# Performance work log

Hardware: AMD Instinct MI355X
Metric: run time of the kernel (lower is better)

The kernel has to match this reference:

```python
import jax, jax.numpy as jnp
import numpy as np

DIM = 512
HEADS = 8
HEAD_DIM = DIM // HEADS
EPS = 1e-6
LN_EPS = 1e-5


def setup_inputs() -> dict:
    key = jax.random.key(0)
    ks = jax.random.split(key, 7)
    B, S = 2, 2048
    std = 1.0 / np.sqrt(DIM)
    return {
        "x": jax.random.normal(ks[0], (B, S, DIM), dtype=jnp.float32),
        "Wq": jax.random.normal(ks[1], (DIM, DIM), dtype=jnp.float32) * std,
        "Wk": jax.random.normal(ks[2], (DIM, DIM), dtype=jnp.float32) * std,
        "Wv": jax.random.normal(ks[3], (DIM, DIM), dtype=jnp.float32) * std,
        "Wo": jax.random.normal(ks[4], (DIM, DIM), dtype=jnp.float32) * std,
        "ln_gamma": jnp.ones((DIM,), dtype=jnp.float32),
        "ln_beta": jnp.zeros((DIM,), dtype=jnp.float32),
    }


def _hardsigmoid(x):
    return jnp.clip(x / 6.0 + 0.5, 0.0, 1.0)


def _softshrink(x, lambd=0.5):
    return jnp.where(x > lambd, x - lambd, jnp.where(x < -lambd, x + lambd, 0.0))


def reference(x, Wq, Wk, Wv, Wo, ln_gamma, ln_beta):
    B, S, D = x.shape
    # torch Linear: y = x @ W.T
    q = (x @ Wq.T).reshape(B, S, HEADS, HEAD_DIM).transpose(0, 2, 1, 3)
    k = (x @ Wk.T).reshape(B, S, HEADS, HEAD_DIM).transpose(0, 2, 1, 3)
    v = (x @ Wv.T).reshape(B, S, HEADS, HEAD_DIM).transpose(0, 2, 1, 3)
    scale = 1.0 / np.sqrt(HEAD_DIM)
    scores = jnp.einsum("bhqd,bhkd->bhqk", q, k) * scale  # [B,H,S,S]
    attn_soft = jax.nn.softmax(scores, axis=-1)
    gated = attn_soft * _hardsigmoid(scores)
    attn_weights = gated / (gated.sum(axis=-1, keepdims=True) + EPS)
    attn_out = jnp.einsum("bhqk,bhkd->bhqd", attn_weights, v)
    attn_out = attn_out.transpose(0, 2, 1, 3).reshape(B, S, D)
    out = attn_out @ Wo.T
    out = out / (1.0 + jnp.abs(out))  # softsign
    out = out + _softshrink(x)
    # LayerNorm over last dim
    mu = out.mean(axis=-1, keepdims=True)
    var = ((out - mu) ** 2).mean(axis=-1, keepdims=True)
    out = (out - mu) * jax.lax.rsqrt(var + LN_EPS) * ln_gamma + ln_beta
    return out
```

## Files before the change

### kernel.cpp

```cpp
#include <hip/hip_runtime.h>

#define DIMD 512
#define NB 2
#define SEQ 2048
#define NHEADS 8
#define HDIM 64
#define MROWS (NB*SEQ)

typedef short s16x8 __attribute__((ext_vector_type(8)));
typedef float f32x4 __attribute__((ext_vector_type(4)));
typedef float f32x16 __attribute__((ext_vector_type(16)));
typedef unsigned short u16;
typedef unsigned int u32;

__device__ __forceinline__ u16 f2bf(float f) {
    union { float f; u32 u; } c; c.f = f;
    u32 u = c.u;
    return (u16)((u + 0x7FFFu + ((u >> 16) & 1u)) >> 16);
}
__device__ __forceinline__ float bf2f(u16 v) {
    union { u32 u; float f; } c; c.u = ((u32)v) << 16;
    return c.f;
}

__device__ __forceinline__ f32x4 mfma16(s16x8 a, s16x8 b, f32x4 c) {
    return __builtin_amdgcn_mfma_f32_16x16x32_bf16(a, b, c, 0, 0, 0);
}
__device__ __forceinline__ f32x16 mfma32(s16x8 a, s16x8 b, f32x16 c) {
    return __builtin_amdgcn_mfma_f32_32x32x16_bf16(a, b, c, 0, 0, 0);
}

#define GLDS16(g, l) __builtin_amdgcn_global_load_lds( \
    (const __attribute__((address_space(1))) void*)(g), \
    (__attribute__((address_space(3))) void*)(l), 16, 0, 0)

#define ESCF 0.180336880111f
#define HSC2 0.115524530f

__global__ void cvt_all(const float* __restrict__ x, const float* __restrict__ Wq,
                        const float* __restrict__ Wk, const float* __restrict__ Wv,
                        const float* __restrict__ Wo,
                        u16* __restrict__ xb, u16* __restrict__ wqkv, u16* __restrict__ wo) {
    int i = blockIdx.x * blockDim.x + threadIdx.x;
    const float* src; u16* dst; int idx;
    if (i < 524288) { src = x; dst = xb; idx = i; }
    else {
        int jj = i - 524288;
        int which = jj >> 16; idx = jj & 65535;
        src = which == 0 ? Wq : which == 1 ? Wk : which == 2 ? Wv : Wo;
        dst = which < 3 ? wqkv + which*DIMD*DIMD : wo;
    }
    float4 v = reinterpret_cast<const float4*>(src)[idx];
    ushort4 o;
    o.x = f2bf(v.x); o.y = f2bf(v.y); o.z = f2bf(v.z); o.w = f2bf(v.w);
    reinterpret_cast<ushort4*>(dst)[idx] = o;
}

template<int WMODE>
__global__ __launch_bounds__(256) void gemm128(const u16* __restrict__ A, const u16* __restrict__ Bm,
                                               void* __restrict__ Cout, void* __restrict__ Cout2,
                                               void* __restrict__ Cout3, int M, int N, int K) {
    __shared__ u16 As[128*64];
    __shared__ u16 Bs[128*64];
    const int bm0 = blockIdx.x * 128, bn0 = blockIdx.y * 128;
    const int t = threadIdx.x;
    const int w = t >> 6, l = t & 63;
    const int lg = l >> 4, lr = l & 15;
    const int wm = w >> 1, wn = w & 1;
    f32x4 acc[4][4] = {};
    const int srow = w*32 + (l >> 3);
    const int swc = ((l & 7) ^ ((l >> 3) & 7)) * 8;
    const u16* asrc = A  + (size_t)(bm0 + srow)*K + swc;
    const u16* bsrc = Bm + (size_t)(bn0 + srow)*K + swc;
    const int ldsb = w*2048;

    for (int k0 = 0; k0 < K; k0 += 64) {
        #pragma unroll
        for (int g = 0; g < 4; g++) {
            GLDS16(asrc + (size_t)g*8*K + k0, &As[ldsb + g*512]);
            GLDS16(bsrc + (size_t)g*8*K + k0, &Bs[ldsb + g*512]);
        }
        __syncthreads();
        #pragma unroll
        for (int ks = 0; ks < 2; ks++) {
            const int swr = ((ks*4 + lg) ^ (lr & 7)) * 8;
            s16x8 af[4], bfr[4];
            #pragma unroll
            for (int fm = 0; fm < 4; fm++)
                af[fm] = *(const s16x8*)&As[(wm*64 + fm*16 + lr)*64 + swr];
            #pragma unroll
            for (int fn = 0; fn < 4; fn++)
                bfr[fn] = *(const s16x8*)&Bs[(wn*64 + fn*16 + lr)*64 + swr];
            #pragma unroll
            for (int fm = 0; fm < 4; fm++)
                #pragma unroll
                for (int fn = 0; fn < 4; fn++)
                    acc[fm][fn] = mfma16(af[fm], bfr[fn], acc[fm][fn]);
        }
        __syncthreads();
    }

    const int region = (WMODE == 3) ? (bn0 >> 9) : 0;
    const float qsc = (WMODE == 3 && region == 0) ? ESCF : 1.0f;
    #pragma unroll
    for (int fm = 0; fm < 4; fm++) {
        #pragma unroll
        for (int fn = 0; fn < 4; fn++) {
            const int mb = bm0 + wm*64 + fm*16 + lg*4;
            const int n  = bn0 + wn*64 + fn*16 + lr;
            if (WMODE == 2) {
                float* C = (float*)Cout;
                #pragma unroll
                for (int i = 0; i < 4; i++)
                    C[(size_t)(mb + i)*N + n] = acc[fm][fn][i];
            } else {
                const int nl = n & 511;
                if (region == 2) {
                    const int b = mb >> 11, s0 = mb & 2047;
                    const int h = nl >> 6, d = nl & 63;
                    ushort4 pk;
                    pk.x = f2bf(acc[fm][fn][0]);
                    pk.y = f2bf(acc[fm][fn][1]);
                    pk.z = f2bf(acc[fm][fn][2]);
                    pk.w = f2bf(acc[fm][fn][3]);
                    *(ushort4*)((u16*)Cout3 + (size_t)((b*8 + h)*64 + d)*2048 + s0) = pk;
                } else {
                    u16* C = region == 0 ? (u16*)Cout : (u16*)Cout2;
                    #pragma unroll
                    for (int i = 0; i < 4; i++)
                        C[(size_t)(mb + i)*512 + nl] = f2bf(acc[fm][fn][i] * qsc);
                }
            }
        }
    }
}

__global__ __launch_bounds__(256) void gemm_bt2(const u16* __restrict__ A, const u16* __restrict__ Bm,
                                                u16* __restrict__ Cout, int M, int N, int K) {
    __shared__ u16 As[64*64];
    __shared__ u16 Bs[64*64];
    const int bm0 = blockIdx.x * 64, bn0 = blockIdx.y * 64;
    const int t = threadIdx.x;
    const int w = t >> 6, l = t & 63;
    const int lg = l >> 4, lr = l & 15;
    const int wm = w >> 1, wn = w & 1;
    f32x4 acc[2][2] = {};
    const int srow = t >> 3;
    const int scol = (t & 7) * 8;

    for (int k0 = 0; k0 < K; k0 += 64) {
        #pragma unroll
        for (int c = 0; c < 2; c++) {
            const u16* ga = A  + (size_t)(bm0 + c*32 + srow)*K + k0 + scol;
            const u16* gb = Bm + (size_t)(bn0 + c*32 + srow)*K + k0 + scol;
            GLDS16(ga, (char*)As + c*4096 + w*1024);
            GLDS16(gb, (char*)Bs + c*4096 + w*1024);
        }
        __syncthreads();
        #pragma unroll
        for (int ks = 0; ks < 2; ks++) {
            s16x8 af[2], bfr[2];
            #pragma unroll
            for (int fm = 0; fm < 2; fm++)
                af[fm] = *(const s16x8*)&As[(wm*32 + fm*16 + lr)*64 + ks*32 + lg*8];
            #pragma unroll
            for (int fn = 0; fn < 2; fn++)
                bfr[fn] = *(const s16x8*)&Bs[(wn*32 + fn*16 + lr)*64 + ks*32 + lg*8];
            #pragma unroll
            for (int fm = 0; fm < 2; fm++)
                #pragma unroll
                for (int fn = 0; fn < 2; fn++)
                    acc[fm][fn] = mfma16(af[fm], bfr[fn], acc[fm][fn]);
        }
        __syncthreads();
    }

    #pragma unroll
    for (int fm = 0; fm < 2; fm++)
        #pragma unroll
        for (int fn = 0; fn < 2; fn++) {
            const int mb = bm0 + wm*32 + fm*16 + lg*4;
            const int n  = bn0 + wn*32 + fn*16 + lr;
            #pragma unroll
            for (int i = 0; i < 4; i++)
                Cout[(size_t)(mb + i)*N + n] = f2bf(acc[fm][fn][i]);
        }
}

__device__ __forceinline__ void attn_phase32(const u16* Kc, const u16* Vc, const s16x8* qf,
                                             f32x16& o0, f32x16& o1, float& gacc,
                                             int ln, int hi, int l7) {
    #pragma unroll
    for (int kb = 0; kb < 4; kb++) {
        f32x16 sc = {};
        __builtin_amdgcn_s_setprio(1);
        #pragma unroll
        for (int c = 0; c < 4; c++) {
            s16x8 kf = *(const s16x8*)&Kc[(kb*32 + ln)*64 + (((c << 1) | hi) ^ l7)*8];
            sc = mfma32(kf, qf[c], sc);
        }
        __builtin_amdgcn_s_setprio(0);
        u32 u[4][2];
        #pragma unroll
        for (int b2 = 0; b2 < 4; b2++) {
            float ww[4];
            #pragma unroll
            for (int r = 0; r < 4; r++) {
                const float s = sc[b2*4 + r];
                const float e = exp2f(s);
                const float hs = __builtin_amdgcn_fmed3f(s*HSC2 + 0.5f, 0.f, 1.f);
                ww[r] = e*hs;
            }
            gacc += (ww[0] + ww[1]) + (ww[2] + ww[3]);
            asm("v_cvt_pk_bf16_f32 %0, %1, %2" : "=v"(u[b2][0]) : "v"(ww[0]), "v"(ww[1]));
            asm("v_cvt_pk_bf16_f32 %0, %1, %2" : "=v"(u[b2][1]) : "v"(ww[2]), "v"(ww[3]));
        }
        #pragma unroll
        for (int c16 = 0; c16 < 2; c16++) {
            u32 x0 = u[2*c16][0], y0 = u[2*c16+1][0];
            u32 x1 = u[2*c16][1], y1 = u[2*c16+1][1];
            asm("v_permlane32_swap_b32 %0, %1" : "+v"(x0), "+v"(y0));
            asm("v_permlane32_swap_b32 %0, %1" : "+v"(x1), "+v"(y1));
            union { u32 uu[4]; s16x8 v; } pa;
            pa.uu[0] = x0; pa.uu[1] = x1; pa.uu[2] = y0; pa.uu[3] = y1;
            const int ccv = kb*4 + c16*2 + hi;
            s16x8 vf0 = *(const s16x8*)&Vc[(size_t)ln*128        + (ccv ^ l7)*8];
            s16x8 vf1 = *(const s16x8*)&Vc[(size_t)(32 + ln)*128 + (ccv ^ l7)*8];
            __builtin_amdgcn_s_setprio(1);
            o0 = mfma32(pa.v, vf0, o0);
            o1 = mfma32(pa.v, vf1, o1);
            __builtin_amdgcn_s_setprio(0);
        }
    }
}

__global__ __launch_bounds__(256) void attn_split(const u16* __restrict__ q, const u16* __restrict__ k,
                                                  const u16* __restrict__ vt,
                                                  float* __restrict__ opart, float* __restrict__ gpart) {
    __shared__ u16 Ks[2][128*64];
    __shared__ u16 Vs[2][64*128];
    const int bid = blockIdx.x;
    const int xcd = bid & 7, j = bid >> 3;
    const int g4 = j >> 4, qt = j & 15;
    const int bhks = xcd*4 + g4;
    const int bh = bhks >> 1, ks = bhks & 1;
    const int b = bh >> 3, h = bh & 7;
    const int qb0 = qt * 128;
    const int t = threadIdx.x;
    const int w = t >> 6, l = t & 63;
    const int ln = l & 31, hi = l >> 5, l7 = l & 7;

    const size_t qrow = (size_t)(b*SEQ + qb0 + w*32 + ln);
    s16x8 qf[4];
    #pragma unroll
    for (int c = 0; c < 4; c++)
        qf[c] = *(const s16x8*)(q + qrow*DIMD + h*HDIM + c*16 + hi*8);

    const int srow = w*32 + (l >> 3);
    const int kswc = (l7 ^ (l >> 3)) * 8;
    const u16* ksrc = k + (size_t)(b*SEQ + ks*1024 + srow)*DIMD + h*HDIM + kswc;
    const u16* vbase = vt + (size_t)bh*HDIM*SEQ + ks*1024;
    int voff[4];
    #pragma unroll
    for (int g = 0; g < 4; g++) {
        const int vrow = w*16 + g*4 + (l >> 4);
        const int vc = ((l & 15) ^ (vrow & 7)) * 8;
        voff[g] = vrow*SEQ + vc;
    }
    const int ldsb = w*2048;

    f32x16 o0 = {}, o1 = {};
    float gacc = 0.f;

    #pragma unroll
    for (int g = 0; g < 4; g++) {
        GLDS16(ksrc + (size_t)g*8*DIMD, &Ks[0][ldsb + g*512]);
        GLDS16(vbase + voff[g],          &Vs[0][ldsb + g*512]);
    }
    __syncthreads();

    #pragma unroll 1
    for (int tp = 0; tp < 4; ++tp) {
        const int tt0 = tp*2;
        {
            const size_t adv = (size_t)(tt0 + 1) * 128;
            #pragma unroll
            for (int g = 0; g < 4; g++) {
                GLDS16(ksrc + (adv + g*8)*DIMD, &Ks[1][ldsb + g*512]);
                GLDS16(vbase + voff[g] + adv,   &Vs[1][ldsb + g*512]);
            }
        }
        attn_phase32(&Ks[0][0], &Vs[0][0], qf, o0, o1, gacc, ln, hi, l7);
        __syncthreads();
        if (tp < 3) {
            const size_t adv = (size_t)(tt0 + 2) * 128;
            #pragma unroll
            for (int g = 0; g < 4; g++) {
                GLDS16(ksrc + (adv + g*8)*DIMD, &Ks[0][ldsb + g*512]);
                GLDS16(vbase + voff[g] + adv,   &Vs[0][ldsb + g*512]);
            }
        }
        attn_phase32(&Ks[1][0], &Vs[1][0], qf, o0, o1, gacc, ln, hi, l7);
        __syncthreads();
    }

    gacc += __shfl_xor(gacc, 32);
    if (l < 32)
        gpart[((size_t)ks*16 + bh)*SEQ + qb0 + w*32 + l] = gacc;

    float* op = opart + ((size_t)ks*MROWS + b*SEQ + qb0 + w*32)*DIMD + h*HDIM;
    #pragma unroll
    for (int i = 0; i < 16; i++) {
        const int qr = (i & 3) + 8*(i >> 2) + 4*hi;
        op[(size_t)qr*DIMD + ln]      = o0[i];
        op[(size_t)qr*DIMD + 32 + ln] = o1[i];
    }
}

__global__ __launch_bounds__(256) void attn_combine(const float* __restrict__ opart,
                                                    const float* __restrict__ gpart,
                                                    u16* __restrict__ attn) {
    const int idx = blockIdx.x*256 + threadIdx.x;
    const int row = idx >> 7;
    const int col = (idx & 127) * 4;
    const int b = row >> 11, s = row & 2047, h = col >> 6;
    const float g = gpart[((size_t)(b*8 + h))*SEQ + s]
                  + gpart[((size_t)(16 + b*8 + h))*SEQ + s];
    const float inv = 1.f / g;
    const float4 a0 = *(const float4*)(opart + (size_t)row*DIMD + col);
    const float4 a1 = *(const float4*)(opart + ((size_t)MROWS + row)*DIMD + col);
    ushort4 r;
    r.x = f2bf((a0.x + a1.x)*inv);
    r.y = f2bf((a0.y + a1.y)*inv);
    r.z = f2bf((a0.z + a1.z)*inv);
    r.w = f2bf((a0.w + a1.w)*inv);
    *(ushort4*)(attn + (size_t)row*DIMD + col) = r;
}

__global__ __launch_bounds__(256) void ln_epilogue(const u16* __restrict__ proj, const float* __restrict__ x,
                                                   const float* __restrict__ gamma, const float* __restrict__ beta,
                                                   float* __restrict__ out) {
    const int row = blockIdx.x*4 + (threadIdx.x >> 6);
    const int l = threadIdx.x & 63;
    const u16* pr = proj + (size_t)row*DIMD + l*8;
    const float* xr = x  + (size_t)row*DIMD + l*8;
    s16x8 pv = *(const s16x8*)pr;
    float tv[8];
    float s = 0.f, s2 = 0.f;
    #pragma unroll
    for (int j = 0; j < 2; j++) {
        float4 xv = *(const float4*)(xr + j*4);
        float xa[4] = {xv.x, xv.y, xv.z, xv.w};
        #pragma unroll
        for (int qq = 0; qq < 4; qq++) {
            const float p = bf2f((u16)pv[j*4+qq]);
            const float ss = p / (1.f + fabsf(p));
            const float xx = xa[qq];
            const float sh = xx > 0.5f ? xx - 0.5f : (xx < -0.5f ? xx + 0.5f : 0.f);
            const float tt = ss + sh;
            tv[j*4+qq] = tt; s += tt; s2 += tt*tt;
        }
    }
    #pragma unroll
    for (int m = 1; m < 64; m <<= 1) { s += __shfl_xor(s, m); s2 += __shfl_xor(s2, m); }
    const float mu = s * (1.f/512.f);
    float var = s2 * (1.f/512.f) - mu*mu;
    const float rstd = rsqrtf(var + 1e-5f);
    #pragma unroll
    for (int j = 0; j < 2; j++) {
        float4 g  = *(const float4*)(gamma + l*8 + j*4);
        float4 bb = *(const float4*)(beta  + l*8 + j*4);
        float4 ov;
        ov.x = (tv[j*4+0]-mu)*rstd*g.x + bb.x;
        ov.y = (tv[j*4+1]-mu)*rstd*g.y + bb.y;
        ov.z = (tv[j*4+2]-mu)*rstd*g.z + bb.z;
        ov.w = (tv[j*4+3]-mu)*rstd*g.w + bb.w;
        *(float4*)(out + (size_t)row*DIMD + l*8 + j*4) = ov;
    }
}

extern "C" void kernel_launch(void* const* d_in, const int* in_sizes, int n_in,
                              void* d_out, int out_size, void* d_ws, size_t ws_size,
                              hipStream_t stream) {
    const float* x     = (const float*)d_in[0];
    const float* Wq    = (const float*)d_in[1];
    const float* Wk    = (const float*)d_in[2];
    const float* Wv    = (const float*)d_in[3];
    const float* Wo    = (const float*)d_in[4];
    const float* gamma = (const float*)d_in[5];
    const float* beta  = (const float*)d_in[6];
    float* out = (float*)d_out;
    char* ws = (char*)d_ws;

    u16* xb    = (u16*)(ws);
    u16* wqkvb = (u16*)(ws + (4<<20));
    u16* wob   = (u16*)(ws + (4<<20) + (1536<<10));
    u16* qb    = (u16*)(ws + (6<<20));
    u16* kb    = (u16*)(ws + (10<<20));
    u16* vtb   = (u16*)(ws + (14<<20));
    u16* ab    = (u16*)(ws + (18<<20));
    u16* proj  = (u16*)(ws + (22<<20));
    float* opart = (float*)(ws + (26<<20));
    float* gpart = (float*)(ws + (42<<20));

    cvt_all<<<3072, 256, 0, stream>>>(x, Wq, Wk, Wv, Wo, xb, wqkvb, wob);

    gemm128<3><<<dim3(MROWS/128, 1536/128), 256, 0, stream>>>(xb, wqkvb, qb, kb, vtb, MROWS, 1536, DIMD);

    attn_split<<<512, 256, 0, stream>>>(qb, kb, vtb, opart, gpart);
    attn_combine<<<2048, 256, 0, stream>>>(opart, gpart, ab);

    gemm_bt2<<<dim3(MROWS/64, DIMD/64), 256, 0, stream>>>(ab, wob, proj, MROWS, DIMD, DIMD);

    ln_epilogue<<<MROWS/4, 256, 0, stream>>>(proj, x, gamma, beta, out);
}
```

Measured before the change: 76.95 us.

## Split attention keys four ways with smaller tiles and bf16 partial outputs

Moves the attention split-K from 2 to 4 key partitions. Each block now processes 512 keys in 64-key tiles, which halves the LDS footprint, and 1024 blocks are launched instead of 512. Partial outputs are stored as bf16 rather than fp32 to cut the write and read traffic into the combine kernel, which now sums four partitions. The aim is more parallelism and occupancy, at the cost of per-block startup overhead, extra partial data to combine, and lower precision in the partial sums.

```diff
diff --git a/kernel.cpp b/kernel.cpp
--- a/kernel.cpp
+++ b/kernel.cpp
@@ -187,11 +187,11 @@
         }
 }
 
-__device__ __forceinline__ void attn_phase32(const u16* Kc, const u16* Vc, const s16x8* qf,
+__device__ __forceinline__ void attn_phase64(const u16* Kc, const u16* Vc, const s16x8* qf,
                                              f32x16& o0, f32x16& o1, float& gacc,
                                              int ln, int hi, int l7) {
     #pragma unroll
-    for (int kb = 0; kb < 4; kb++) {
+    for (int kb = 0; kb < 2; kb++) {
         f32x16 sc = {};
         __builtin_amdgcn_s_setprio(1);
         #pragma unroll
@@ -224,8 +224,8 @@
             union { u32 uu[4]; s16x8 v; } pa;
             pa.uu[0] = x0; pa.uu[1] = x1; pa.uu[2] = y0; pa.uu[3] = y1;
             const int ccv = kb*4 + c16*2 + hi;
-            s16x8 vf0 = *(const s16x8*)&Vc[(size_t)ln*128        + (ccv ^ l7)*8];
-            s16x8 vf1 = *(const s16x8*)&Vc[(size_t)(32 + ln)*128 + (ccv ^ l7)*8];
+            s16x8 vf0 = *(const s16x8*)&Vc[(size_t)ln*64        + (ccv ^ l7)*8];
+            s16x8 vf1 = *(const s16x8*)&Vc[(size_t)(32 + ln)*64 + (ccv ^ l7)*8];
             __builtin_amdgcn_s_setprio(1);
             o0 = mfma32(pa.v, vf0, o0);
             o1 = mfma32(pa.v, vf1, o1);
@@ -236,14 +236,14 @@
 
 __global__ __launch_bounds__(256) void attn_split(const u16* __restrict__ q, const u16* __restrict__ k,
                                                   const u16* __restrict__ vt,
-                                                  float* __restrict__ opart, float* __restrict__ gpart) {
-    __shared__ u16 Ks[2][128*64];
-    __shared__ u16 Vs[2][64*128];
+                                                  u16* __restrict__ opart, float* __restrict__ gpart) {
+    __shared__ u16 Ks[2][64*64];
+    __shared__ u16 Vs[2][64*64];
     const int bid = blockIdx.x;
     const int xcd = bid & 7, j = bid >> 3;
-    const int g4 = j >> 4, qt = j & 15;
-    const int bhks = xcd*4 + g4;
-    const int bh = bhks >> 1, ks = bhks & 1;
+    const int g8 = j >> 4, qt = j & 15;
+    const int bhks = xcd*8 + g8;
+    const int bh = bhks >> 2, ks = bhks & 3;
     const int b = bh >> 3, h = bh & 7;
     const int qb0 = qt * 128;
     const int t = threadIdx.x;
@@ -256,26 +256,19 @@
     for (int c = 0; c < 4; c++)
         qf[c] = *(const s16x8*)(q + qrow*DIMD + h*HDIM + c*16 + hi*8);
 
-    const int srow = w*32 + (l >> 3);
-    const int kswc = (l7 ^ (l >> 3)) * 8;
-    const u16* ksrc = k + (size_t)(b*SEQ + ks*1024 + srow)*DIMD + h*HDIM + kswc;
-    const u16* vbase = vt + (size_t)bh*HDIM*SEQ + ks*1024;
-    int voff[4];
-    #pragma unroll
-    for (int g = 0; g < 4; g++) {
-        const int vrow = w*16 + g*4 + (l >> 4);
-        const int vc = ((l & 15) ^ (vrow & 7)) * 8;
-        voff[g] = vrow*SEQ + vc;
-    }
-    const int ldsb = w*2048;
+    const int sr = l >> 3;
+    const int swc = ((l & 7) ^ sr) * 8;
+    const u16* ksrc = k  + (size_t)(b*SEQ + ks*512 + w*16 + sr)*DIMD + h*HDIM + swc;
+    const u16* vsrc = vt + (size_t)bh*HDIM*SEQ + (size_t)(w*16 + sr)*SEQ + ks*512 + swc;
+    const int ldsw = w*1024;
 
     f32x16 o0 = {}, o1 = {};
     float gacc = 0.f;
 
     #pragma unroll
-    for (int g = 0; g < 4; g++) {
-        GLDS16(ksrc + (size_t)g*8*DIMD, &Ks[0][ldsb + g*512]);
-        GLDS16(vbase + voff[g],          &Vs[0][ldsb + g*512]);
+    for (int g = 0; g < 2; g++) {
+        GLDS16(ksrc + (size_t)g*8*DIMD, &Ks[0][ldsw + g*512]);
+        GLDS16(vsrc + (size_t)g*8*SEQ,  &Vs[0][ldsw + g*512]);
     }
     __syncthreads();
 
@@ -283,24 +276,24 @@
     for (int tp = 0; tp < 4; ++tp) {
         const int tt0 = tp*2;
         {
-            const size_t adv = (size_t)(tt0 + 1) * 128;
-            #pragma unroll
-            for (int g = 0; g < 4; g++) {
-                GLDS16(ksrc + (adv + g*8)*DIMD, &Ks[1][ldsb + g*512]);
-                GLDS16(vbase + voff[g] + adv,   &Vs[1][ldsb + g*512]);
+            const int adv = (tt0 + 1) * 64;
+            #pragma unroll
+            for (int g = 0; g < 2; g++) {
+                GLDS16(ksrc + (size_t)(adv)*DIMD + (size_t)g*8*DIMD, &Ks[1][ldsw + g*512]);
+                GLDS16(vsrc + (size_t)g*8*SEQ + adv,                 &Vs[1][ldsw + g*512]);
             }
         }
-        attn_phase32(&Ks[0][0], &Vs[0][0], qf, o0, o1, gacc, ln, hi, l7);
+        attn_phase64(&Ks[0][0], &Vs[0][0], qf, o0, o1, gacc, ln, hi, l7);
         __syncthreads();
         if (tp < 3) {
-            const size_t adv = (size_t)(tt0 + 2) * 128;
-            #pragma unroll
-            for (int g = 0; g < 4; g++) {
-                GLDS16(ksrc + (adv + g*8)*DIMD, &Ks[0][ldsb + g*512]);
-                GLDS16(vbase + voff[g] + adv,   &Vs[0][ldsb + g*512]);
+            const int adv = (tt0 + 2) * 64;
+            #pragma unroll
+            for (int g = 0; g < 2; g++) {
+                GLDS16(ksrc + (size_t)(adv)*DIMD + (size_t)g*8*DIMD, &Ks[0][ldsw + g*512]);
+                GLDS16(vsrc + (size_t)g*8*SEQ + adv,                 &Vs[0][ldsw + g*512]);
             }
         }
-        attn_phase32(&Ks[1][0], &Vs[1][0], qf, o0, o1, gacc, ln, hi, l7);
+        attn_phase64(&Ks[1][0], &Vs[1][0], qf, o0, o1, gacc, ln, hi, l7);
         __syncthreads();
     }
 
@@ -308,33 +301,38 @@
     if (l < 32)
         gpart[((size_t)ks*16 + bh)*SEQ + qb0 + w*32 + l] = gacc;
 
-    float* op = opart + ((size_t)ks*MROWS + b*SEQ + qb0 + w*32)*DIMD + h*HDIM;
+    u16* op = opart + ((size_t)ks*MROWS + b*SEQ + qb0 + w*32)*DIMD + h*HDIM;
     #pragma unroll
     for (int i = 0; i < 16; i++) {
         const int qr = (i & 3) + 8*(i >> 2) + 4*hi;
-        op[(size_t)qr*DIMD + ln]      = o0[i];
-        op[(size_t)qr*DIMD + 32 + ln] = o1[i];
-    }
-}
-
-__global__ __launch_bounds__(256) void attn_combine(const float* __restrict__ opart,
+        op[(size_t)qr*DIMD + ln]      = f2bf(o0[i]);
+        op[(size_t)qr*DIMD + 32 + ln] = f2bf(o1[i]);
+    }
+}
+
+__global__ __launch_bounds__(256) void attn_combine(const u16* __restrict__ opart,
                                                     const float* __restrict__ gpart,
                                                     u16* __restrict__ attn) {
     const int idx = blockIdx.x*256 + threadIdx.x;
-    const int row = idx >> 7;
-    const int col = (idx & 127) * 4;
-    const int b = row >> 11, s = row & 2047, h = col >> 6;
-    const float g = gpart[((size_t)(b*8 + h))*SEQ + s]
-                  + gpart[((size_t)(16 + b*8 + h))*SEQ + s];
+    const int row = idx >> 6;
+    const int colb = (idx & 63) * 8;
+    const int b = row >> 11, s = row & 2047, h = colb >> 6;
+    float g = 0.f;
+    #pragma unroll
+    for (int p = 0; p < 4; p++)
+        g += gpart[((size_t)p*16 + b*8 + h)*SEQ + s];
     const float inv = 1.f / g;
-    const float4 a0 = *(const float4*)(opart + (size_t)row*DIMD + col);
-    const float4 a1 = *(const float4*)(opart + ((size_t)MROWS + row)*DIMD + col);
-    ushort4 r;
-    r.x = f2bf((a0.x + a1.x)*inv);
-    r.y = f2bf((a0.y + a1.y)*inv);
-    r.z = f2bf((a0.z + a1.z)*inv);
-    r.w = f2bf((a0.w + a1.w)*inv);
-    *(ushort4*)(attn + (size_t)row*DIMD + col) = r;
+    float acc[8] = {};
+    #pragma unroll
+    for (int p = 0; p < 4; p++) {
+        s16x8 v = *(const s16x8*)(opart + ((size_t)p*MROWS + row)*DIMD + colb);
+        #pragma unroll
+        for (int j2 = 0; j2 < 8; j2++) acc[j2] += bf2f((u16)v[j2]);
+    }
+    union { u16 r[8]; s16x8 v; } o;
+    #pragma unroll
+    for (int j2 = 0; j2 < 8; j2++) o.r[j2] = f2bf(acc[j2]*inv);
+    *(s16x8*)(attn + (size_t)row*DIMD + colb) = o.v;
 }
 
 __global__ __launch_bounds__(256) void ln_epilogue(const u16* __restrict__ proj, const float* __restrict__ x,
@@ -400,15 +398,15 @@
     u16* vtb   = (u16*)(ws + (14<<20));
     u16* ab    = (u16*)(ws + (18<<20));
     u16* proj  = (u16*)(ws + (22<<20));
-    float* opart = (float*)(ws + (26<<20));
+    u16* opart = (u16*)(ws + (26<<20));
     float* gpart = (float*)(ws + (42<<20));
 
     cvt_all<<<3072, 256, 0, stream>>>(x, Wq, Wk, Wv, Wo, xb, wqkvb, wob);
 
     gemm128<3><<<dim3(MROWS/128, 1536/128), 256, 0, stream>>>(xb, wqkvb, qb, kb, vtb, MROWS, 1536, DIMD);
 
-    attn_split<<<512, 256, 0, stream>>>(qb, kb, vtb, opart, gpart);
-    attn_combine<<<2048, 256, 0, stream>>>(opart, gpart, ab);
+    attn_split<<<1024, 256, 0, stream>>>(qb, kb, vtb, opart, gpart);
+    attn_combine<<<1024, 256, 0, stream>>>(opart, gpart, ab);
 
     gemm_bt2<<<dim3(MROWS/64, DIMD/64), 256, 0, stream>>>(ab, wob, proj, MROWS, DIMD, DIMD);
 
```

After: 76.42 us. No clear change (-0.7%).
